# Kernel optimization log

Measured on AMD Instinct MI355X. Metric: run time of the kernel, lower is better.

Reference implementation:

```python
import jax, jax.numpy as jnp
import numpy as np
from jax import lax

CLIP = 1.0  # STE clip value for both input and kernel quantizers
EPS = 1e-3  # keras BatchNormalization default epsilon

@jax.custom_vjp
def binarize(x):
    # sign with >=0 -> +1, <0 -> -1 (matches tf.where(x>=0, 1, -1))
    return jnp.where(x >= 0, jnp.ones_like(x), -jnp.ones_like(x))

def _bin_fwd(x):
    return binarize(x), x

def _bin_bwd(x, g):
    # straight-through estimator: pass grad where |x| <= clip, else 0
    return (jnp.where(jnp.abs(x) <= CLIP, g, jnp.zeros_like(g)),)

binarize.defvjp(_bin_fwd, _bin_bwd)

def setup_inputs() -> dict:
    key = jax.random.key(0)
    k1, k2, k3 = jax.random.split(key, 3)
    B, H, Wd, C = 32, 56, 56, 128
    x = jax.random.normal(k1, (B, H, Wd, C), dtype=jnp.float32)
    W = jax.random.normal(k2, (3, 3, C, C), dtype=jnp.float32) * 0.05  # HWIO
    gamma = jnp.ones((C,), dtype=jnp.float32) + 0.1 * jax.random.normal(k3, (C,), dtype=jnp.float32)
    beta = jnp.zeros((C,), dtype=jnp.float32)
    return {"x": x, "W": W, "gamma": gamma, "beta": beta}

def reference(x, W, gamma, beta):
    # binarize activations and weights (sign with STE grad)
    xb = binarize(x)
    wb = binarize(W)
    # 3x3 SAME conv, stride 1, NHWC / HWIO
    y = lax.conv_general_dilated(
        xb, wb, window_strides=(1, 1), padding='SAME',
        dimension_numbers=('NHWC', 'HWIO', 'NHWC'))
    r = jax.nn.relu(y)
    # training-mode batch norm over axes (0,1,2)
    mean = jnp.mean(r, axis=(0, 1, 2), keepdims=True)
    var = jnp.var(r, axis=(0, 1, 2), keepdims=True)
    r_std = (r - mean) * lax.rsqrt(var + EPS)
    out_bn = gamma * r_std + beta
    # shortcut add with (un-binarized) input
    return out_bn + x
```

## Files before the change

### kernel.cpp

```cpp
#include <hip/hip_runtime.h>

#define CH    128
#define HH    56
#define WW    56
#define BB    32
#define NPIX  (BB * HH * WW)
#define NSLOT 16

#define XROW   7424
#define XBATCH 430592
#define LDSROW 8448
#define SWZ(pl, ci) ((ci) ^ (((pl) & 7) << 4))

typedef int i32x4  __attribute__((ext_vector_type(4)));
typedef int i32x16 __attribute__((ext_vector_type(16)));

__device__ __forceinline__ void mfma_i8(i32x16& acc, i32x4 a, i32x4 b) {
    asm("v_mfma_i32_32x32x32_i8 %0, %1, %2, %0" : "+v"(acc) : "v"(a), "v"(b));
}

__global__ __launch_bounds__(256) void prep_k(const float* __restrict__ x,
                                              const float* __restrict__ Wt,
                                              signed char* __restrict__ xi8,
                                              signed char* __restrict__ wfrag,
                                              unsigned long long* __restrict__ accum) {
    int bx = blockIdx.x, tid = threadIdx.x;
    if (bx < 12544) {
        int t = bx * 256 + tid;
        int p = t >> 5;
        int ci0 = (t & 31) * 4;
        int w = p % WW;
        int t2 = p / WW;
        int h = t2 % HH;
        int b = t2 / HH;
        float4 v = ((const float4*)x)[t];
        unsigned o = (v.x >= 0.f ? 0x01u : 0xFFu)
                   | ((v.y >= 0.f ? 0x01u : 0xFFu) << 8)
                   | ((v.z >= 0.f ? 0x01u : 0xFFu) << 16)
                   | ((v.w >= 0.f ? 0x01u : 0xFFu) << 24);
        *(unsigned*)(xi8 + (size_t)b * XBATCH + (size_t)(h + 1) * XROW + (w + 1) * 128 + ci0) = o;
    } else if (bx < 12772) {
        int c = (bx - 12544) * 256 + tid;
        int cell = c >> 3, q = c & 7;
        int b = cell / 228, e = cell % 228;
        int row, col;
        if (e < 58)       { row = 0;       col = e; }
        else if (e < 116) { row = 57;      col = e - 58; }
        else if (e < 172) { row = e - 115; col = 0; }
        else              { row = e - 171; col = 57; }
        i32x4 z = {0, 0, 0, 0};
        *(i32x4*)(xi8 + (size_t)b * XBATCH + (size_t)row * XROW + col * 128 + q * 16) = z;
    } else if (bx < 12808) {
        int i = (bx - 12772) * 256 + tid;
        int n = i / 2304;
        int r = i % 2304;
        int q = r / 64;
        int L = r % 64;
        int tap = q >> 2, kk = q & 3;
        int co = 32 * n + (L & 31);
        int kbase = 32 * kk + (L >> 5) * 16;
        i32x4 o;
        #pragma unroll
        for (int d = 0; d < 4; ++d) {
            unsigned u = 0;
            #pragma unroll
            for (int by = 0; by < 4; ++by) {
                int ci = kbase + 4 * d + by;
                unsigned s = (Wt[((size_t)tap * 128 + ci) * 128 + co] >= 0.f) ? 0x01u : 0xFFu;
                u |= s << (8 * by);
            }
            o[d] = (int)u;
        }
        *(i32x4*)(wfrag + (size_t)i * 16) = o;
    } else {
        for (int k = tid; k < NSLOT * 256; k += 256) accum[k] = 0ull;
    }
}

__global__ __launch_bounds__(512) void gemm1_k(const signed char* __restrict__ xi8,
                                               const signed char* __restrict__ wfrag,
                                               unsigned long long* __restrict__ accum) {
    __shared__ alignas(16) char sm[4 * LDSROW];

    int ph0 = 1 + ((blockIdx.x * 7) % HH);
    int b   = (blockIdx.x * 7) / HH;

    int L = threadIdx.x & 63, w = threadIdx.x >> 6;
    int n32 = w & 3, sh = w >> 2;
    int l31 = L & 31, hi = L >> 5;

    int coff[3][4];
    #pragma unroll
    for (int dw = 0; dw < 3; ++dw) {
        int pld = l31 + dw;
        int pl = 32 * sh + pld;
        #pragma unroll
        for (int kk = 0; kk < 4; ++kk)
            coff[dw][kk] = pl * 128 + ((32 * kk + 16 * hi) ^ ((pld & 7) << 4));
    }

    const i32x4* bfp = (const i32x4*)wfrag + (size_t)n32 * 36 * 64;
    i32x4 bfr[36];
    #pragma unroll
    for (int q = 0; q < 36; ++q) bfr[q] = bfp[q * 64 + L];

    int co = 32 * n32 + l31;

    for (int c = threadIdx.x; c < 1392; c += 512) {
        int rr = c / 464;
        int off = (c % 464) * 16;
        int row = ph0 - 1 + rr;
        int p = off >> 7, ci0 = off & 127;
        i32x4 v = *(const i32x4*)(xi8 + (size_t)b * XBATCH + (size_t)row * XROW + off);
        int pl = p + 1;
        *(i32x4*)(sm + (row & 3) * LDSROW + pl * 128 + SWZ(pl, ci0)) = v;
    }
    if (threadIdx.x < 256) {
        int slot = threadIdx.x >> 6, g = threadIdx.x & 63;
        int gp = g >> 3, ci0 = (g & 7) * 16;
        int pl = (gp == 0) ? 0 : (58 + gp);
        i32x4 z = {0, 0, 0, 0};
        *(i32x4*)(sm + slot * LDSROW + pl * 128 + SWZ(pl, ci0)) = z;
    }
    __syncthreads();

    #pragma unroll 1
    for (int t = 0; t < 7; ++t) {
        int ph = ph0 + t;
        int id = blockIdx.x * 7 + t;

        i32x4 stv;
        int stdst = -1;
        if (t < 6 && threadIdx.x < 464) {
            int nrow = ph + 2;
            int off = threadIdx.x * 16;
            int p = off >> 7, ci0 = off & 127;
            stv = *(const i32x4*)(xi8 + (size_t)b * XBATCH + (size_t)nrow * XROW + off);
            int pl = p + 1;
            stdst = (nrow & 3) * LDSROW + pl * 128 + SWZ(pl, ci0);
        }

        int rs[3] = { ((ph - 1) & 3) * LDSROW, (ph & 3) * LDSROW, ((ph + 1) & 3) * LDSROW };

        i32x16 acc0 = {}, acc1 = {};
        #pragma unroll
        for (int q = 0; q < 36; ++q) {
            int tap = q >> 2, kk = q & 3;
            int dh = tap / 3, dw = tap % 3;
            i32x4 a = *(const i32x4*)(sm + rs[dh] + coff[dw][kk]);
            if (q & 1) mfma_i8(acc1, a, bfr[q]);
            else       mfma_i8(acc0, a, bfr[q]);
        }
        asm volatile("s_nop 7\n\ts_nop 7\n\ts_nop 7" : "+v"(acc0), "+v"(acc1));
        #pragma unroll
        for (int e = 0; e < 16; ++e) acc0[e] += acc1[e];

        unsigned s1 = 0, s2 = 0;
        #pragma unroll
        for (int reg = 0; reg < 16; ++reg) {
            int pw = 32 * sh + (reg & 3) + 8 * (reg >> 2) + 4 * hi;
            int y = acc0[reg];
            int r = y > 0 ? y : 0;
            if (pw >= 1 && pw <= WW) {
                s1 += (unsigned)r;
                s2 += (unsigned)__mul24(r, r);
            }
        }
        s1 += __shfl_xor(s1, 32);
        s2 += __shfl_xor(s2, 32);
        if (hi == 0) {
            int slot = id & (NSLOT - 1);
            atomicAdd(&accum[slot * 256 + co],       (unsigned long long)s1);
            atomicAdd(&accum[slot * 256 + 128 + co], (unsigned long long)s2);
        }

        if (stdst >= 0) *(i32x4*)(sm + stdst) = stv;
        __syncthreads();
    }
}

__global__ __launch_bounds__(512) void gemm2_k(const signed char* __restrict__ xi8,
                                               const signed char* __restrict__ wfrag,
                                               const unsigned long long* __restrict__ accum,
                                               const float* __restrict__ gamma,
                                               const float* __restrict__ beta,
                                               const float* __restrict__ x,
                                               float* __restrict__ out) {
    __shared__ alignas(16) char sm[4 * LDSROW];
    __shared__ unsigned short r_lds[WW * CH];
    __shared__ float2 ssl[CH];

    int ph0 = 1 + ((blockIdx.x * 7) % HH);
    int b   = (blockIdx.x * 7) / HH;

    int L = threadIdx.x & 63, w = threadIdx.x >> 6;
    int n32 = w & 3, sh = w >> 2;
    int l31 = L & 31, hi = L >> 5;

    int coff[3][4];
    #pragma unroll
    for (int dw = 0; dw < 3; ++dw) {
        int pld = l31 + dw;
        int pl = 32 * sh + pld;
        #pragma unroll
        for (int kk = 0; kk < 4; ++kk)
            coff[dw][kk] = pl * 128 + ((32 * kk + 16 * hi) ^ ((pld & 7) << 4));
    }

    const i32x4* bfp = (const i32x4*)wfrag + (size_t)n32 * 36 * 64;
    i32x4 bfr[36];
    #pragma unroll
    for (int q = 0; q < 36; ++q) bfr[q] = bfp[q * 64 + L];

    int co = 32 * n32 + l31;

    for (int c = threadIdx.x; c < 1392; c += 512) {
        int rr = c / 464;
        int off = (c % 464) * 16;
        int row = ph0 - 1 + rr;
        int p = off >> 7, ci0 = off & 127;
        i32x4 v = *(const i32x4*)(xi8 + (size_t)b * XBATCH + (size_t)row * XROW + off);
        int pl = p + 1;
        *(i32x4*)(sm + (row & 3) * LDSROW + pl * 128 + SWZ(pl, ci0)) = v;
    }
    if (threadIdx.x < 256) {
        int slot = threadIdx.x >> 6, g = threadIdx.x & 63;
        int gp = g >> 3, ci0 = (g & 7) * 16;
        int pl = (gp == 0) ? 0 : (58 + gp);
        i32x4 z = {0, 0, 0, 0};
        *(i32x4*)(sm + slot * LDSROW + pl * 128 + SWZ(pl, ci0)) = z;
    }
    if (threadIdx.x < CH) {
        int c = threadIdx.x;
        unsigned long long a1 = 0, a2 = 0;
        #pragma unroll
        for (int s = 0; s < NSLOT; ++s) {
            a1 += accum[s * 256 + c];
            a2 += accum[s * 256 + 128 + c];
        }
        float N    = (float)NPIX;
        float mean = (float)a1 / N;
        float ex2  = (float)a2 / N;
        float var  = fmaf(-mean, mean, ex2);
        float rstd = 1.0f / sqrtf(var + 1e-3f);
        float sc   = gamma[c] * rstd;
        float2 v;
        v.x = sc;
        v.y = fmaf(-mean, sc, beta[c]);
        ssl[c] = v;
    }
    __syncthreads();

    int c40 = (threadIdx.x & 31) * 4;
    float2 t0 = ssl[c40 + 0], t1 = ssl[c40 + 1];
    float2 t2 = ssl[c40 + 2], t3 = ssl[c40 + 3];

    #pragma unroll 1
    for (int t = 0; t < 7; ++t) {
        int ph = ph0 + t;

        i32x4 stv;
        int stdst = -1;
        if (t < 6 && threadIdx.x < 464) {
            int nrow = ph + 2;
            int off = threadIdx.x * 16;
            int p = off >> 7, ci0 = off & 127;
            stv = *(const i32x4*)(xi8 + (size_t)b * XBATCH + (size_t)nrow * XROW + off);
            int pl = p + 1;
            stdst = (nrow & 3) * LDSROW + pl * 128 + SWZ(pl, ci0);
        }

        int rs[3] = { ((ph - 1) & 3) * LDSROW, (ph & 3) * LDSROW, ((ph + 1) & 3) * LDSROW };

        i32x16 acc0 = {}, acc1 = {};
        #pragma unroll
        for (int q = 0; q < 36; ++q) {
            int tap = q >> 2, kk = q & 3;
            int dh = tap / 3, dw = tap % 3;
            i32x4 a = *(const i32x4*)(sm + rs[dh] + coff[dw][kk]);
            if (q & 1) mfma_i8(acc1, a, bfr[q]);
            else       mfma_i8(acc0, a, bfr[q]);
        }
        asm volatile("s_nop 7\n\ts_nop 7\n\ts_nop 7" : "+v"(acc0), "+v"(acc1));
        #pragma unroll
        for (int e = 0; e < 16; ++e) acc0[e] += acc1[e];

        #pragma unroll
        for (int reg = 0; reg < 16; ++reg) {
            int pw = 32 * sh + (reg & 3) + 8 * (reg >> 2) + 4 * hi;
            int y = acc0[reg];
            if (pw >= 1 && pw <= WW)
                r_lds[(pw - 1) * CH + co] = (unsigned short)(y > 0 ? y : 0);
        }
        __syncthreads();

        size_t row4 = (size_t)(b * HH + ph - 1) * (WW * CH / 4);
        for (int i = threadIdx.x; i < WW * CH / 4; i += 512) {
            ushort4 rv = ((const ushort4*)r_lds)[i];
            float4 xv = ((const float4*)x)[row4 + i];
            float4 o;
            o.x = fmaf((float)rv.x, t0.x, t0.y + xv.x);
            o.y = fmaf((float)rv.y, t1.x, t1.y + xv.y);
            o.z = fmaf((float)rv.z, t2.x, t2.y + xv.z);
            o.w = fmaf((float)rv.w, t3.x, t3.y + xv.w);
            ((float4*)out)[row4 + i] = o;
        }

        if (stdst >= 0) *(i32x4*)(sm + stdst) = stv;
        __syncthreads();
    }
}

extern "C" void kernel_launch(void* const* d_in, const int* in_sizes, int n_in,
                              void* d_out, int out_size, void* d_ws, size_t ws_size,
                              hipStream_t stream) {
    const float* x     = (const float*)d_in[0];
    const float* Wt    = (const float*)d_in[1];
    const float* gamma = (const float*)d_in[2];
    const float* beta  = (const float*)d_in[3];
    float* out = (float*)d_out;
    char* ws = (char*)d_ws;

    signed char* xi8   = (signed char*)ws;
    signed char* wfrag = (signed char*)(ws + 13778944);
    unsigned long long* accum = (unsigned long long*)(ws + 13926400);

    hipLaunchKernelGGL(prep_k,  dim3(12809), dim3(256), 0, stream, x, Wt, xi8, wfrag, accum);
    hipLaunchKernelGGL(gemm1_k, dim3(256),   dim3(512), 0, stream, xi8, wfrag, accum);
    hipLaunchKernelGGL(gemm2_k, dim3(256),   dim3(512), 0, stream, xi8, wfrag, accum,
                       gamma, beta, x, out);
}
```

Measured before the change: 68.67 us.

## Use planar LDS layout, prefetch residual x, double-buffer epilogue to drop a barrier

The XOR-swizzled LDS layout for the int8 activation rows is replaced by a channel-plane layout: eight planes of 16-byte groups per row. The residual x row in gemm2 is now loaded into registers before the MFMA loop, so its global latency overlaps the convolution math. The ReLU staging buffer is double-buffered, which lets the per-row loop use one barrier instead of two. Launch bounds now give occupancy hints (1 and 2 blocks). The cost is more registers and LDS, plus possible bank conflicts from the new plane stride.

```diff
diff --git a/kernel.cpp b/kernel.cpp
--- a/kernel.cpp
+++ b/kernel.cpp
@@ -10,7 +10,8 @@
 #define XROW   7424
 #define XBATCH 430592
 #define LDSROW 8448
-#define SWZ(pl, ci) ((ci) ^ (((pl) & 7) << 4))
+#define PLANE  1056
+#define ROW4   (WW * CH / 4)
 
 typedef int i32x4  __attribute__((ext_vector_type(4)));
 typedef int i32x16 __attribute__((ext_vector_type(16)));
@@ -77,9 +78,9 @@
     }
 }
 
-__global__ __launch_bounds__(512) void gemm1_k(const signed char* __restrict__ xi8,
-                                               const signed char* __restrict__ wfrag,
-                                               unsigned long long* __restrict__ accum) {
+__global__ __launch_bounds__(512, 1) void gemm1_k(const signed char* __restrict__ xi8,
+                                                  const signed char* __restrict__ wfrag,
+                                                  unsigned long long* __restrict__ accum) {
     __shared__ alignas(16) char sm[4 * LDSROW];
 
     int ph0 = 1 + ((blockIdx.x * 7) % HH);
@@ -92,11 +93,10 @@
     int coff[3][4];
     #pragma unroll
     for (int dw = 0; dw < 3; ++dw) {
-        int pld = l31 + dw;
-        int pl = 32 * sh + pld;
+        int px = 32 * sh + l31 + dw;
         #pragma unroll
         for (int kk = 0; kk < 4; ++kk)
-            coff[dw][kk] = pl * 128 + ((32 * kk + 16 * hi) ^ ((pld & 7) << 4));
+            coff[dw][kk] = (2 * kk + hi) * PLANE + px * 16;
     }
 
     const i32x4* bfp = (const i32x4*)wfrag + (size_t)n32 * 36 * 64;
@@ -108,19 +108,17 @@
 
     for (int c = threadIdx.x; c < 1392; c += 512) {
         int rr = c / 464;
-        int off = (c % 464) * 16;
+        int cc = c % 464;
         int row = ph0 - 1 + rr;
-        int p = off >> 7, ci0 = off & 127;
-        i32x4 v = *(const i32x4*)(xi8 + (size_t)b * XBATCH + (size_t)row * XROW + off);
-        int pl = p + 1;
-        *(i32x4*)(sm + (row & 3) * LDSROW + pl * 128 + SWZ(pl, ci0)) = v;
+        i32x4 v = *(const i32x4*)(xi8 + (size_t)b * XBATCH + (size_t)row * XROW + cc * 16);
+        *(i32x4*)(sm + (row & 3) * LDSROW + (cc & 7) * PLANE + ((cc >> 3) + 1) * 16) = v;
     }
     if (threadIdx.x < 256) {
         int slot = threadIdx.x >> 6, g = threadIdx.x & 63;
-        int gp = g >> 3, ci0 = (g & 7) * 16;
+        int plane = g >> 3, gp = g & 7;
         int pl = (gp == 0) ? 0 : (58 + gp);
         i32x4 z = {0, 0, 0, 0};
-        *(i32x4*)(sm + slot * LDSROW + pl * 128 + SWZ(pl, ci0)) = z;
+        *(i32x4*)(sm + slot * LDSROW + plane * PLANE + pl * 16) = z;
     }
     __syncthreads();
 
@@ -133,11 +131,9 @@
         int stdst = -1;
         if (t < 6 && threadIdx.x < 464) {
             int nrow = ph + 2;
-            int off = threadIdx.x * 16;
-            int p = off >> 7, ci0 = off & 127;
-            stv = *(const i32x4*)(xi8 + (size_t)b * XBATCH + (size_t)nrow * XROW + off);
-            int pl = p + 1;
-            stdst = (nrow & 3) * LDSROW + pl * 128 + SWZ(pl, ci0);
+            int cc = threadIdx.x;
+            stv = *(const i32x4*)(xi8 + (size_t)b * XBATCH + (size_t)nrow * XROW + cc * 16);
+            stdst = (nrow & 3) * LDSROW + (cc & 7) * PLANE + ((cc >> 3) + 1) * 16;
         }
 
         int rs[3] = { ((ph - 1) & 3) * LDSROW, (ph & 3) * LDSROW, ((ph + 1) & 3) * LDSROW };
@@ -179,15 +175,15 @@
     }
 }
 
-__global__ __launch_bounds__(512) void gemm2_k(const signed char* __restrict__ xi8,
-                                               const signed char* __restrict__ wfrag,
-                                               const unsigned long long* __restrict__ accum,
-                                               const float* __restrict__ gamma,
-                                               const float* __restrict__ beta,
-                                               const float* __restrict__ x,
-                                               float* __restrict__ out) {
+__global__ __launch_bounds__(512, 2) void gemm2_k(const signed char* __restrict__ xi8,
+                                                  const signed char* __restrict__ wfrag,
+                                                  const unsigned long long* __restrict__ accum,
+                                                  const float* __restrict__ gamma,
+                                                  const float* __restrict__ beta,
+                                                  const float* __restrict__ x,
+                                                  float* __restrict__ out) {
     __shared__ alignas(16) char sm[4 * LDSROW];
-    __shared__ unsigned short r_lds[WW * CH];
+    __shared__ unsigned short r_lds[2][WW * CH];
     __shared__ float2 ssl[CH];
 
     int ph0 = 1 + ((blockIdx.x * 7) % HH);
@@ -200,11 +196,10 @@
     int coff[3][4];
     #pragma unroll
     for (int dw = 0; dw < 3; ++dw) {
-        int pld = l31 + dw;
-        int pl = 32 * sh + pld;
+        int px = 32 * sh + l31 + dw;
         #pragma unroll
         for (int kk = 0; kk < 4; ++kk)
-            coff[dw][kk] = pl * 128 + ((32 * kk + 16 * hi) ^ ((pld & 7) << 4));
+            coff[dw][kk] = (2 * kk + hi) * PLANE + px * 16;
     }
 
     const i32x4* bfp = (const i32x4*)wfrag + (size_t)n32 * 36 * 64;
@@ -216,19 +211,17 @@
 
     for (int c = threadIdx.x; c < 1392; c += 512) {
         int rr = c / 464;
-        int off = (c % 464) * 16;
+        int cc = c % 464;
         int row = ph0 - 1 + rr;
-        int p = off >> 7, ci0 = off & 127;
-        i32x4 v = *(const i32x4*)(xi8 + (size_t)b * XBATCH + (size_t)row * XROW + off);
-        int pl = p + 1;
-        *(i32x4*)(sm + (row & 3) * LDSROW + pl * 128 + SWZ(pl, ci0)) = v;
+        i32x4 v = *(const i32x4*)(xi8 + (size_t)b * XBATCH + (size_t)row * XROW + cc * 16);
+        *(i32x4*)(sm + (row & 3) * LDSROW + (cc & 7) * PLANE + ((cc >> 3) + 1) * 16) = v;
     }
     if (threadIdx.x < 256) {
         int slot = threadIdx.x >> 6, g = threadIdx.x & 63;
-        int gp = g >> 3, ci0 = (g & 7) * 16;
+        int plane = g >> 3, gp = g & 7;
         int pl = (gp == 0) ? 0 : (58 + gp);
         i32x4 z = {0, 0, 0, 0};
-        *(i32x4*)(sm + slot * LDSROW + pl * 128 + SWZ(pl, ci0)) = z;
+        *(i32x4*)(sm + slot * LDSROW + plane * PLANE + pl * 16) = z;
     }
     if (threadIdx.x < CH) {
         int c = threadIdx.x;
@@ -258,16 +251,21 @@
     #pragma unroll 1
     for (int t = 0; t < 7; ++t) {
         int ph = ph0 + t;
-
+        size_t row4 = (size_t)(b * HH + ph - 1) * ROW4;
+
+        float4 xreg[4];
+        #pragma unroll
+        for (int k = 0; k < 4; ++k) {
+            int i = threadIdx.x + k * 512;
+            if (i < ROW4) xreg[k] = ((const float4*)x)[row4 + i];
+        }
         i32x4 stv;
         int stdst = -1;
         if (t < 6 && threadIdx.x < 464) {
             int nrow = ph + 2;
-            int off = threadIdx.x * 16;
-            int p = off >> 7, ci0 = off & 127;
-            stv = *(const i32x4*)(xi8 + (size_t)b * XBATCH + (size_t)nrow * XROW + off);
-            int pl = p + 1;
-            stdst = (nrow & 3) * LDSROW + pl * 128 + SWZ(pl, ci0);
+            int cc = threadIdx.x;
+            stv = *(const i32x4*)(xi8 + (size_t)b * XBATCH + (size_t)nrow * XROW + cc * 16);
+            stdst = (nrow & 3) * LDSROW + (cc & 7) * PLANE + ((cc >> 3) + 1) * 16;
         }
 
         int rs[3] = { ((ph - 1) & 3) * LDSROW, (ph & 3) * LDSROW, ((ph + 1) & 3) * LDSROW };
@@ -285,29 +283,31 @@
         #pragma unroll
         for (int e = 0; e < 16; ++e) acc0[e] += acc1[e];
 
+        unsigned short* rl = r_lds[t & 1];
         #pragma unroll
         for (int reg = 0; reg < 16; ++reg) {
             int pw = 32 * sh + (reg & 3) + 8 * (reg >> 2) + 4 * hi;
             int y = acc0[reg];
             if (pw >= 1 && pw <= WW)
-                r_lds[(pw - 1) * CH + co] = (unsigned short)(y > 0 ? y : 0);
-        }
+                rl[(pw - 1) * CH + co] = (unsigned short)(y > 0 ? y : 0);
+        }
+        if (stdst >= 0) *(i32x4*)(sm + stdst) = stv;
+
         __syncthreads();
 
-        size_t row4 = (size_t)(b * HH + ph - 1) * (WW * CH / 4);
-        for (int i = threadIdx.x; i < WW * CH / 4; i += 512) {
-            ushort4 rv = ((const ushort4*)r_lds)[i];
-            float4 xv = ((const float4*)x)[row4 + i];
-            float4 o;
-            o.x = fmaf((float)rv.x, t0.x, t0.y + xv.x);
-            o.y = fmaf((float)rv.y, t1.x, t1.y + xv.y);
-            o.z = fmaf((float)rv.z, t2.x, t2.y + xv.z);
-            o.w = fmaf((float)rv.w, t3.x, t3.y + xv.w);
-            ((float4*)out)[row4 + i] = o;
-        }
-
-        if (stdst >= 0) *(i32x4*)(sm + stdst) = stv;
-        __syncthreads();
+        #pragma unroll
+        for (int k = 0; k < 4; ++k) {
+            int i = threadIdx.x + k * 512;
+            if (i < ROW4) {
+                ushort4 rv = ((const ushort4*)rl)[i];
+                float4 o;
+                o.x = fmaf((float)rv.x, t0.x, t0.y + xreg[k].x);
+                o.y = fmaf((float)rv.y, t1.x, t1.y + xreg[k].y);
+                o.z = fmaf((float)rv.z, t2.x, t2.y + xreg[k].z);
+                o.w = fmaf((float)rv.w, t3.x, t3.y + xreg[k].w);
+                ((float4*)out)[row4 + i] = o;
+            }
+        }
     }
 }
 
```

Measured after the change: 63.58 us. 1.08x faster.
